# Optimization experiments

Hardware: AMD Instinct MI355X
Metric: run time of the kernel (lower is better)

The kernel has to match this reference:

```python
import jax, jax.numpy as jnp
from jax import lax
import numpy as np

STATE_DIM, LATENT_DIM, HIDDEN_DIM = 18, 3, 16
BN_EPS = 1e-5


def _xavier(key, out_dim, in_dim):
    a = (6.0 / (in_dim + out_dim)) ** 0.5
    return jax.random.uniform(key, (out_dim, in_dim), minval=-a, maxval=a, dtype=jnp.float32)


def setup_inputs() -> dict:
    key = jax.random.key(0)
    ks = jax.random.split(key, 12)
    B, S, T = 4096, 256, 64
    inp = {
        "x_sequence": jax.random.normal(ks[0], (B, S, STATE_DIM), dtype=jnp.float32),
        "t_span": jnp.linspace(0.0, 6.3, T, dtype=jnp.float32),
        # encoder: Linear(18->16), ReLU, (Dropout off), BatchNorm1d(16, eval), Linear(16->3)
        "enc_w1": _xavier(ks[1], HIDDEN_DIM, STATE_DIM), "enc_b1": jnp.zeros((HIDDEN_DIM,), jnp.float32),
        "enc_bn_g": jnp.ones((HIDDEN_DIM,), jnp.float32), "enc_bn_b": jnp.zeros((HIDDEN_DIM,), jnp.float32),
        "enc_bn_m": jnp.zeros((HIDDEN_DIM,), jnp.float32), "enc_bn_v": jnp.ones((HIDDEN_DIM,), jnp.float32),
        "enc_w2": _xavier(ks[2], LATENT_DIM, HIDDEN_DIM), "enc_b2": jnp.zeros((LATENT_DIM,), jnp.float32),
        # decoder: Linear(3->16), ReLU, BN(16, eval), Linear(16->18)
        "dec_w1": _xavier(ks[3], HIDDEN_DIM, LATENT_DIM), "dec_b1": jnp.zeros((HIDDEN_DIM,), jnp.float32),
        "dec_bn_g": jnp.ones((HIDDEN_DIM,), jnp.float32), "dec_bn_b": jnp.zeros((HIDDEN_DIM,), jnp.float32),
        "dec_bn_m": jnp.zeros((HIDDEN_DIM,), jnp.float32), "dec_bn_v": jnp.ones((HIDDEN_DIM,), jnp.float32),
        "dec_w2": _xavier(ks[4], STATE_DIM, HIDDEN_DIM), "dec_b2": jnp.zeros((STATE_DIM,), jnp.float32),
        # ode_func: Linear(3->8), Tanh, Linear(8->3)
        "ode_w1": _xavier(ks[5], HIDDEN_DIM // 2, LATENT_DIM), "ode_b1": jnp.zeros((HIDDEN_DIM // 2,), jnp.float32),
        "ode_w2": _xavier(ks[6], LATENT_DIM, HIDDEN_DIM // 2), "ode_b2": jnp.zeros((LATENT_DIM,), jnp.float32),
        # perturbation classifier: Linear(3->4), ReLU, Linear(4->1), Sigmoid
        "cls_w1": _xavier(ks[7], 4, LATENT_DIM), "cls_b1": jnp.zeros((4,), jnp.float32),
        "cls_w2": _xavier(ks[8], 1, 4), "cls_b2": jnp.zeros((1,), jnp.float32),
    }
    return inp


def _bn_eval(x, g, b, m, v):
    return (x - m) * (g / jnp.sqrt(v + BN_EPS)) + b


def reference(x_sequence, t_span,
              enc_w1, enc_b1, enc_bn_g, enc_bn_b, enc_bn_m, enc_bn_v, enc_w2, enc_b2,
              dec_w1, dec_b1, dec_bn_g, dec_bn_b, dec_bn_m, dec_bn_v, dec_w2, dec_b2,
              ode_w1, ode_b1, ode_w2, ode_b2,
              cls_w1, cls_b1, cls_w2, cls_b2):
    B, S, D = x_sequence.shape
    T = t_span.shape[0]

    def encode(x):  # [N, 18] -> [N, 3]
        h = jax.nn.relu(x @ enc_w1.T + enc_b1)
        h = _bn_eval(h, enc_bn_g, enc_bn_b, enc_bn_m, enc_bn_v)
        return h @ enc_w2.T + enc_b2

    def decode(z):  # [N, 3] -> [N, 18]
        h = jax.nn.relu(z @ dec_w1.T + dec_b1)
        h = _bn_eval(h, dec_bn_g, dec_bn_b, dec_bn_m, dec_bn_v)
        return h @ dec_w2.T + dec_b2

    def ode_func(z):  # [B, 3] -> [B, 3]
        return jnp.tanh(z @ ode_w1.T + ode_b1) @ ode_w2.T + ode_b2

    x_flat = x_sequence.reshape(-1, D)              # [B*S, 18]
    z_flat = encode(x_flat)                         # [B*S, 3]
    z_seq = z_flat.reshape(B, S, LATENT_DIM)
    z0 = z_seq[:, -1, :]                            # [B, 3]

    # explicit Euler integration: z <- z + 0.1 * f(z), T steps
    def step(z, _):
        z_next = z + 0.1 * ode_func(z)
        return z_next, z_next

    _, z_traj = lax.scan(step, z0, None, length=T)  # [T, B, 3]
    z_pred = jnp.transpose(z_traj, (1, 0, 2))       # [B, T, 3]

    x_recon = decode(z_flat).reshape(B, S, D)
    x_pred = decode(z_pred.reshape(-1, LATENT_DIM)).reshape(B, T, D)

    z_mean = jnp.mean(z_seq, axis=1)                # [B, 3]
    h = jax.nn.relu(z_mean @ cls_w1.T + cls_b1)
    perturbation_prob = jax.nn.sigmoid(h @ cls_w2.T + cls_b2)  # [B, 1]

    return (x_recon, x_pred, perturbation_prob, z_seq)
```

## Files before the change

kernel.cpp:

```cpp
#include <hip/hip_runtime.h>
#include <math.h>

constexpr int Bn = 4096, Sn = 256, Tn = 64;
constexpr int Dn = 18, Hn = 16, Ln = 3;
constexpr float EPS = 1e-5f;
constexpr int R = 4;

constexpr size_t OFF_XP   = (size_t)Bn * Sn * Dn;
constexpr size_t OFF_PROB = OFF_XP + (size_t)Bn * Tn * Dn;
constexpr size_t OFF_ZS   = OFF_PROB + (size_t)Bn;

__device__ __forceinline__ float fast_tanh(float x) {
    float ax = fabsf(x);
    float e  = __expf(-2.0f * ax);
    float r  = (1.0f - e) / (1.0f + e);
    return copysignf(r, x);
}

__global__ __launch_bounds__(256) void k1_encdec(
    const float* __restrict__ x,
    const float* __restrict__ ew1, const float* __restrict__ eb1,
    const float* __restrict__ eg,  const float* __restrict__ ebb,
    const float* __restrict__ em,  const float* __restrict__ ev,
    const float* __restrict__ ew2, const float* __restrict__ eb2,
    const float* __restrict__ dw1, const float* __restrict__ db1,
    const float* __restrict__ dg,  const float* __restrict__ dbn,
    const float* __restrict__ dm,  const float* __restrict__ dv,
    const float* __restrict__ dw2, const float* __restrict__ db2,
    const float* __restrict__ cw1, const float* __restrict__ cb1,
    const float* __restrict__ cw2, const float* __restrict__ cb2,
    float* __restrict__ xrec, float* __restrict__ prob, float* __restrict__ zseq)
{
    const int s = threadIdx.x;
    const size_t row0 = (size_t)blockIdx.x * (R * Sn) + s;

    float h[R][Hn];
    #pragma unroll
    for (int j = 0; j < Hn; ++j) {
        float b = eb1[j];
        #pragma unroll
        for (int r = 0; r < R; ++r) h[r][j] = b;
    }
    #pragma unroll
    for (int kk = 0; kk < Dn / 2; ++kk) {
        float2 xa[R];
        #pragma unroll
        for (int r = 0; r < R; ++r)
            xa[r] = *reinterpret_cast<const float2*>(x + (row0 + (size_t)r * Sn) * Dn + 2 * kk);
        #pragma unroll
        for (int j = 0; j < Hn; ++j) {
            float w0 = ew1[j * Dn + 2 * kk];
            float w1 = ew1[j * Dn + 2 * kk + 1];
            #pragma unroll
            for (int r = 0; r < R; ++r) {
                h[r][j] = fmaf(w0, xa[r].x, h[r][j]);
                h[r][j] = fmaf(w1, xa[r].y, h[r][j]);
            }
        }
    }
    #pragma unroll
    for (int j = 0; j < Hn; ++j) {
        float sc = eg[j] / sqrtf(ev[j] + EPS);
        float sh = ebb[j] - em[j] * sc;
        #pragma unroll
        for (int r = 0; r < R; ++r)
            h[r][j] = fmaf(fmaxf(h[r][j], 0.0f), sc, sh);
    }

    float zz[R][Ln];
    #pragma unroll
    for (int c = 0; c < Ln; ++c) {
        float b = eb2[c];
        #pragma unroll
        for (int r = 0; r < R; ++r) zz[r][c] = b;
    }
    #pragma unroll
    for (int j = 0; j < Hn; ++j) {
        #pragma unroll
        for (int c = 0; c < Ln; ++c) {
            float w = ew2[c * Hn + j];
            #pragma unroll
            for (int r = 0; r < R; ++r) zz[r][c] = fmaf(w, h[r][j], zz[r][c]);
        }
    }
    #pragma unroll
    for (int r = 0; r < R; ++r) {
        float* zp = zseq + (row0 + (size_t)r * Sn) * Ln;
        zp[0] = zz[r][0]; zp[1] = zz[r][1]; zp[2] = zz[r][2];
    }

    float h2[R][Hn];
    #pragma unroll
    for (int j = 0; j < Hn; ++j) {
        float w0 = dw1[j * Ln + 0], w1 = dw1[j * Ln + 1], w2 = dw1[j * Ln + 2];
        float b  = db1[j];
        float sc = dg[j] / sqrtf(dv[j] + EPS);
        float sh = dbn[j] - dm[j] * sc;
        #pragma unroll
        for (int r = 0; r < R; ++r) {
            float a = fmaf(w0, zz[r][0], b);
            a = fmaf(w1, zz[r][1], a);
            a = fmaf(w2, zz[r][2], a);
            h2[r][j] = fmaf(fmaxf(a, 0.0f), sc, sh);
        }
    }
    #pragma unroll
    for (int m = 0; m < Dn; m += 2) {
        float o0[R], o1[R];
        #pragma unroll
        for (int r = 0; r < R; ++r) { o0[r] = db2[m]; o1[r] = db2[m + 1]; }
        #pragma unroll
        for (int j = 0; j < Hn; ++j) {
            float wa = dw2[m * Hn + j];
            float wb = dw2[(m + 1) * Hn + j];
            #pragma unroll
            for (int r = 0; r < R; ++r) {
                o0[r] = fmaf(wa, h2[r][j], o0[r]);
                o1[r] = fmaf(wb, h2[r][j], o1[r]);
            }
        }
        #pragma unroll
        for (int r = 0; r < R; ++r)
            *reinterpret_cast<float2*>(xrec + (row0 + (size_t)r * Sn) * Dn + m) =
                make_float2(o0[r], o1[r]);
    }

    float acc[R][Ln];
    #pragma unroll
    for (int r = 0; r < R; ++r)
        #pragma unroll
        for (int c = 0; c < Ln; ++c) acc[r][c] = zz[r][c];
    #pragma unroll
    for (int off = 32; off > 0; off >>= 1) {
        #pragma unroll
        for (int r = 0; r < R; ++r)
            #pragma unroll
            for (int c = 0; c < Ln; ++c)
                acc[r][c] += __shfl_down(acc[r][c], off);
    }
    __shared__ float red[4][R][Ln];
    const int lane = s & 63, wid = s >> 6;
    if (lane == 0) {
        #pragma unroll
        for (int r = 0; r < R; ++r)
            #pragma unroll
            for (int c = 0; c < Ln; ++c) red[wid][r][c] = acc[r][c];
    }
    __syncthreads();
    if (s < R) {
        float m0 = (red[0][s][0] + red[1][s][0] + red[2][s][0] + red[3][s][0]) * (1.0f / Sn);
        float m1 = (red[0][s][1] + red[1][s][1] + red[2][s][1] + red[3][s][1]) * (1.0f / Sn);
        float m2 = (red[0][s][2] + red[1][s][2] + red[2][s][2] + red[3][s][2]) * (1.0f / Sn);
        float logit = cb2[0];
        #pragma unroll
        for (int j = 0; j < 4; ++j) {
            float a = fmaf(cw1[j * 3 + 0], m0, cb1[j]);
            a = fmaf(cw1[j * 3 + 1], m1, a);
            a = fmaf(cw1[j * 3 + 2], m2, a);
            a = fmaxf(a, 0.0f);
            logit = fmaf(cw2[j], a, logit);
        }
        prob[blockIdx.x * R + s] = 1.0f / (1.0f + __expf(-logit));
    }
}

__global__ __launch_bounds__(64) void k2_ode(
    const float* __restrict__ zseq,
    const float* __restrict__ ow1, const float* __restrict__ ob1,
    const float* __restrict__ ow2, const float* __restrict__ ob2,
    float* __restrict__ zscr, int zlayout)
{
    const int b = blockIdx.x * blockDim.x + threadIdx.x;
    const float* zp = zseq + ((size_t)b * Sn + (Sn - 1)) * Ln;
    float z0 = zp[0], z1 = zp[1], z2 = zp[2];

    float w1[8][3], bb1[8], w2v[3][8], bb2[3];
    #pragma unroll
    for (int j = 0; j < 8; ++j) {
        bb1[j] = ob1[j];
        #pragma unroll
        for (int k = 0; k < 3; ++k) w1[j][k] = ow1[j * 3 + k];
    }
    #pragma unroll
    for (int i = 0; i < 3; ++i) {
        bb2[i] = ob2[i];
        #pragma unroll
        for (int j = 0; j < 8; ++j) w2v[i][j] = ow2[i * 8 + j];
    }

    for (int t = 0; t < Tn; ++t) {
        float a[8];
        #pragma unroll
        for (int j = 0; j < 8; ++j) {
            float u = fmaf(w1[j][0], z0, bb1[j]);
            u = fmaf(w1[j][1], z1, u);
            u = fmaf(w1[j][2], z2, u);
            a[j] = fast_tanh(u);
        }
        float d0 = bb2[0], d1 = bb2[1], d2 = bb2[2];
        #pragma unroll
        for (int j = 0; j < 8; ++j) {
            d0 = fmaf(w2v[0][j], a[j], d0);
            d1 = fmaf(w2v[1][j], a[j], d1);
            d2 = fmaf(w2v[2][j], a[j], d2);
        }
        z0 = fmaf(0.1f, d0, z0);
        z1 = fmaf(0.1f, d1, z1);
        z2 = fmaf(0.1f, d2, z2);
        size_t idx = (zlayout == 0) ? ((size_t)t * Bn + b) * Ln
                                    : ((size_t)b * Tn + t) * Dn;
        zscr[idx + 0] = z0; zscr[idx + 1] = z1; zscr[idx + 2] = z2;
    }
}

__global__ __launch_bounds__(256) void k3_decpred(
    const float* __restrict__ dw1, const float* __restrict__ db1,
    const float* __restrict__ dg,  const float* __restrict__ dbn,
    const float* __restrict__ dm,  const float* __restrict__ dv,
    const float* __restrict__ dw2, const float* __restrict__ db2,
    const float* __restrict__ zscr, int zlayout,
    float* __restrict__ xpred)
{
    const int s = threadIdx.x;
    const size_t row0 = (size_t)blockIdx.x * (R * 256) + s;

    float zz[R][Ln];
    #pragma unroll
    for (int r = 0; r < R; ++r) {
        size_t row = row0 + (size_t)r * 256;
        size_t zidx = (zlayout == 0) ? (((row & 63) * Bn + (row >> 6)) * Ln)
                                     : row * Dn;
        zz[r][0] = zscr[zidx + 0];
        zz[r][1] = zscr[zidx + 1];
        zz[r][2] = zscr[zidx + 2];
    }

    float h2[R][Hn];
    #pragma unroll
    for (int j = 0; j < Hn; ++j) {
        float w0 = dw1[j * Ln + 0], w1 = dw1[j * Ln + 1], w2 = dw1[j * Ln + 2];
        float b  = db1[j];
        float sc = dg[j] / sqrtf(dv[j] + EPS);
        float sh = dbn[j] - dm[j] * sc;
        #pragma unroll
        for (int r = 0; r < R; ++r) {
            float a = fmaf(w0, zz[r][0], b);
            a = fmaf(w1, zz[r][1], a);
            a = fmaf(w2, zz[r][2], a);
            h2[r][j] = fmaf(fmaxf(a, 0.0f), sc, sh);
        }
    }
    #pragma unroll
    for (int m = 0; m < Dn; m += 2) {
        float o0[R], o1[R];
        #pragma unroll
        for (int r = 0; r < R; ++r) { o0[r] = db2[m]; o1[r] = db2[m + 1]; }
        #pragma unroll
        for (int j = 0; j < Hn; ++j) {
            float wa = dw2[m * Hn + j];
            float wb = dw2[(m + 1) * Hn + j];
            #pragma unroll
            for (int r = 0; r < R; ++r) {
                o0[r] = fmaf(wa, h2[r][j], o0[r]);
                o1[r] = fmaf(wb, h2[r][j], o1[r]);
            }
        }
        #pragma unroll
        for (int r = 0; r < R; ++r)
            *reinterpret_cast<float2*>(xpred + (row0 + (size_t)r * 256) * Dn + m) =
                make_float2(o0[r], o1[r]);
    }
}

extern "C" void kernel_launch(void* const* d_in, const int* in_sizes, int n_in,
                              void* d_out, int out_size, void* d_ws, size_t ws_size,
                              hipStream_t stream)
{
    const float* x   = (const float*)d_in[0];
    const float* ew1 = (const float*)d_in[2];
    const float* eb1 = (const float*)d_in[3];
    const float* eg  = (const float*)d_in[4];
    const float* ebb = (const float*)d_in[5];
    const float* em  = (const float*)d_in[6];
    const float* ev  = (const float*)d_in[7];
    const float* ew2 = (const float*)d_in[8];
    const float* eb2 = (const float*)d_in[9];
    const float* dw1 = (const float*)d_in[10];
    const float* db1 = (const float*)d_in[11];
    const float* dg  = (const float*)d_in[12];
    const float* dbn = (const float*)d_in[13];
    const float* dm  = (const float*)d_in[14];
    const float* dv  = (const float*)d_in[15];
    const float* dw2 = (const float*)d_in[16];
    const float* db2 = (const float*)d_in[17];
    const float* ow1 = (const float*)d_in[18];
    const float* ob1 = (const float*)d_in[19];
    const float* ow2 = (const float*)d_in[20];
    const float* ob2 = (const float*)d_in[21];
    const float* cw1 = (const float*)d_in[22];
    const float* cb1 = (const float*)d_in[23];
    const float* cw2 = (const float*)d_in[24];
    const float* cb2 = (const float*)d_in[25];

    float* out   = (float*)d_out;
    float* xrec  = out;
    float* xpred = out + OFF_XP;
    float* prob  = out + OFF_PROB;
    float* zseq  = out + OFF_ZS;

    const size_t zbytes = (size_t)Bn * Tn * Ln * sizeof(float);
    float* zscr; int zlayout;
    if (ws_size >= zbytes) { zscr = (float*)d_ws; zlayout = 0; }
    else                   { zscr = xpred;        zlayout = 1; }

    k1_encdec<<<dim3(Bn / R), dim3(Sn), 0, stream>>>(
        x, ew1, eb1, eg, ebb, em, ev, ew2, eb2,
        dw1, db1, dg, dbn, dm, dv, dw2, db2,
        cw1, cb1, cw2, cb2, xrec, prob, zseq);

    k2_ode<<<dim3(Bn / 64), dim3(64), 0, stream>>>(
        zseq, ow1, ob1, ow2, ob2, zscr, zlayout);

    k3_decpred<<<dim3((Bn * Tn) / (R * 256)), dim3(256), 0, stream>>>(
        dw1, db1, dg, dbn, dm, dv, dw2, db2, zscr, zlayout, xpred);
}
```

Baseline: 293.3 us.

## Stage input and output tiles through LDS for coalesced float4 global access

The encoder kernel now loads its whole 4x256x18 input tile into shared memory with coalesced float4 reads. It computes from LDS, writes the reconstruction back into the same buffer, and stores it with coalesced float4 writes. The predicted-decode kernel likewise stages its outputs in LDS before a float4 store. The z scratch layout becomes batch-major with a stride, so the ODE writes and decoder reads are contiguous per row. The cost is about 72KB of LDS per block, which limits occupancy, plus bank conflicts on the stride-18 LDS accesses.

```diff
diff --git a/kernel.cpp b/kernel.cpp
--- a/kernel.cpp
+++ b/kernel.cpp
@@ -32,7 +32,19 @@
     float* __restrict__ xrec, float* __restrict__ prob, float* __restrict__ zseq)
 {
     const int s = threadIdx.x;
-    const size_t row0 = (size_t)blockIdx.x * (R * Sn) + s;
+    constexpr int TILE_F   = Sn * Dn;
+    constexpr int TILE4_F  = R * TILE_F;
+    constexpr int TILE4_F4 = TILE4_F / 4;
+
+    __shared__ float xt[TILE4_F];
+    __shared__ float red[4][R][Ln];
+
+    const size_t base = (size_t)blockIdx.x * TILE4_F;
+    const float4* xg  = reinterpret_cast<const float4*>(x + base);
+    float4*       xt4 = reinterpret_cast<float4*>(xt);
+    #pragma unroll 4
+    for (int i = s; i < TILE4_F4; i += 256) xt4[i] = xg[i];
+    __syncthreads();
 
     float h[R][Hn];
     #pragma unroll
@@ -46,7 +58,7 @@
         float2 xa[R];
         #pragma unroll
         for (int r = 0; r < R; ++r)
-            xa[r] = *reinterpret_cast<const float2*>(x + (row0 + (size_t)r * Sn) * Dn + 2 * kk);
+            xa[r] = *reinterpret_cast<const float2*>(&xt[r * TILE_F + s * Dn + 2 * kk]);
         #pragma unroll
         for (int j = 0; j < Hn; ++j) {
             float w0 = ew1[j * Dn + 2 * kk];
@@ -85,7 +97,7 @@
     }
     #pragma unroll
     for (int r = 0; r < R; ++r) {
-        float* zp = zseq + (row0 + (size_t)r * Sn) * Ln;
+        float* zp = zseq + (((size_t)blockIdx.x * R + r) * Sn + s) * Ln;
         zp[0] = zz[r][0]; zp[1] = zz[r][1]; zp[2] = zz[r][2];
     }
 
@@ -120,10 +132,16 @@
             }
         }
         #pragma unroll
-        for (int r = 0; r < R; ++r)
-            *reinterpret_cast<float2*>(xrec + (row0 + (size_t)r * Sn) * Dn + m) =
-                make_float2(o0[r], o1[r]);
-    }
+        for (int r = 0; r < R; ++r) {
+            xt[r * TILE_F + s * Dn + m]     = o0[r];
+            xt[r * TILE_F + s * Dn + m + 1] = o1[r];
+        }
+    }
+    __syncthreads();
+
+    float4* og = reinterpret_cast<float4*>(xrec + base);
+    #pragma unroll 4
+    for (int i = s; i < TILE4_F4; i += 256) og[i] = xt4[i];
 
     float acc[R][Ln];
     #pragma unroll
@@ -138,7 +156,6 @@
             for (int c = 0; c < Ln; ++c)
                 acc[r][c] += __shfl_down(acc[r][c], off);
     }
-    __shared__ float red[4][R][Ln];
     const int lane = s & 63, wid = s >> 6;
     if (lane == 0) {
         #pragma unroll
@@ -168,7 +185,7 @@
     const float* __restrict__ zseq,
     const float* __restrict__ ow1, const float* __restrict__ ob1,
     const float* __restrict__ ow2, const float* __restrict__ ob2,
-    float* __restrict__ zscr, int zlayout)
+    float* __restrict__ zscr, int zstride)
 {
     const int b = blockIdx.x * blockDim.x + threadIdx.x;
     const float* zp = zseq + ((size_t)b * Sn + (Sn - 1)) * Ln;
@@ -188,6 +205,7 @@
         for (int j = 0; j < 8; ++j) w2v[i][j] = ow2[i * 8 + j];
     }
 
+    float* op = zscr + (size_t)b * Tn * zstride;
     for (int t = 0; t < Tn; ++t) {
         float a[8];
         #pragma unroll
@@ -207,9 +225,7 @@
         z0 = fmaf(0.1f, d0, z0);
         z1 = fmaf(0.1f, d1, z1);
         z2 = fmaf(0.1f, d2, z2);
-        size_t idx = (zlayout == 0) ? ((size_t)t * Bn + b) * Ln
-                                    : ((size_t)b * Tn + t) * Dn;
-        zscr[idx + 0] = z0; zscr[idx + 1] = z1; zscr[idx + 2] = z2;
+        op[t * zstride + 0] = z0; op[t * zstride + 1] = z1; op[t * zstride + 2] = z2;
     }
 }
 
@@ -218,18 +234,22 @@
     const float* __restrict__ dg,  const float* __restrict__ dbn,
     const float* __restrict__ dm,  const float* __restrict__ dv,
     const float* __restrict__ dw2, const float* __restrict__ db2,
-    const float* __restrict__ zscr, int zlayout,
+    const float* __restrict__ zscr, int zstride,
     float* __restrict__ xpred)
 {
     const int s = threadIdx.x;
-    const size_t row0 = (size_t)blockIdx.x * (R * 256) + s;
+    constexpr int ROWS    = R * 256;
+    constexpr int TILE_F  = ROWS * Dn;
+    constexpr int TILE_F4 = TILE_F / 4;
+
+    __shared__ float ot[TILE_F];
+
+    const size_t row0 = (size_t)blockIdx.x * ROWS + s;
 
     float zz[R][Ln];
     #pragma unroll
     for (int r = 0; r < R; ++r) {
-        size_t row = row0 + (size_t)r * 256;
-        size_t zidx = (zlayout == 0) ? (((row & 63) * Bn + (row >> 6)) * Ln)
-                                     : row * Dn;
+        size_t zidx = (row0 + (size_t)r * 256) * zstride;
         zz[r][0] = zscr[zidx + 0];
         zz[r][1] = zscr[zidx + 1];
         zz[r][2] = zscr[zidx + 2];
@@ -266,10 +286,17 @@
             }
         }
         #pragma unroll
-        for (int r = 0; r < R; ++r)
-            *reinterpret_cast<float2*>(xpred + (row0 + (size_t)r * 256) * Dn + m) =
-                make_float2(o0[r], o1[r]);
-    }
+        for (int r = 0; r < R; ++r) {
+            ot[(r * 256 + s) * Dn + m]     = o0[r];
+            ot[(r * 256 + s) * Dn + m + 1] = o1[r];
+        }
+    }
+    __syncthreads();
+
+    float4* og = reinterpret_cast<float4*>(xpred + (size_t)blockIdx.x * TILE_F);
+    const float4* ot4 = reinterpret_cast<const float4*>(ot);
+    #pragma unroll 4
+    for (int i = s; i < TILE_F4; i += 256) og[i] = ot4[i];
 }
 
 extern "C" void kernel_launch(void* const* d_in, const int* in_sizes, int n_in,
@@ -309,9 +336,9 @@
     float* zseq  = out + OFF_ZS;
 
     const size_t zbytes = (size_t)Bn * Tn * Ln * sizeof(float);
-    float* zscr; int zlayout;
-    if (ws_size >= zbytes) { zscr = (float*)d_ws; zlayout = 0; }
-    else                   { zscr = xpred;        zlayout = 1; }
+    float* zscr; int zstride;
+    if (ws_size >= zbytes) { zscr = (float*)d_ws; zstride = Ln; }
+    else                   { zscr = xpred;        zstride = Dn; }
 
     k1_encdec<<<dim3(Bn / R), dim3(Sn), 0, stream>>>(
         x, ew1, eb1, eg, ebb, em, ev, ew2, eb2,
@@ -319,8 +346,8 @@
         cw1, cb1, cw2, cb2, xrec, prob, zseq);
 
     k2_ode<<<dim3(Bn / 64), dim3(64), 0, stream>>>(
-        zseq, ow1, ob1, ow2, ob2, zscr, zlayout);
+        zseq, ow1, ob1, ow2, ob2, zscr, zstride);
 
     k3_decpred<<<dim3((Bn * Tn) / (R * 256)), dim3(256), 0, stream>>>(
-        dw1, db1, dg, dbn, dm, dv, dw2, db2, zscr, zlayout, xpred);
-}
+        dw1, db1, dg, dbn, dm, dv, dw2, db2, zscr, zstride, xpred);
+}
```

Measured after the change: 273.0 us. -6.9%, faster.

## Give each thread four consecutive rows with float4 loads and stores

Applied to the files above, without the earlier changes.

The encoder/decoder kernels now assign four contiguous rows to each thread instead of rows strided by 256. This lets each thread load and store its 72-float row group with float4 vector accesses. The ODE scratch layout changes to batch-major so the predicted-trajectory decoder can also read latents with float4 loads. Loops are reordered to fuse the hidden layer into the output accumulation, and the classifier reduction now uses one wavefront per batch element with no shared memory or barrier. The trade-off is much higher register pressure from 72-element input and output arrays, plus per-lane accesses strided by 288 bytes within a wavefront, which may hurt occupancy and coalescing.

```diff
diff --git a/kernel.cpp b/kernel.cpp
--- a/kernel.cpp
+++ b/kernel.cpp
@@ -4,11 +4,12 @@
 constexpr int Bn = 4096, Sn = 256, Tn = 64;
 constexpr int Dn = 18, Hn = 16, Ln = 3;
 constexpr float EPS = 1e-5f;
-constexpr int R = 4;
 
 constexpr size_t OFF_XP   = (size_t)Bn * Sn * Dn;
 constexpr size_t OFF_PROB = OFF_XP + (size_t)Bn * Tn * Dn;
 constexpr size_t OFF_ZS   = OFF_PROB + (size_t)Bn;
+
+#define OF(e) out_[(e) / Dn][(e) % Dn]
 
 __device__ __forceinline__ float fast_tanh(float x) {
     float ax = fabsf(x);
@@ -32,125 +33,102 @@
     float* __restrict__ xrec, float* __restrict__ prob, float* __restrict__ zseq)
 {
     const int s = threadIdx.x;
-    const size_t row0 = (size_t)blockIdx.x * (R * Sn) + s;
-
-    float h[R][Hn];
-    #pragma unroll
-    for (int j = 0; j < Hn; ++j) {
-        float b = eb1[j];
-        #pragma unroll
-        for (int r = 0; r < R; ++r) h[r][j] = b;
-    }
-    #pragma unroll
-    for (int kk = 0; kk < Dn / 2; ++kk) {
-        float2 xa[R];
-        #pragma unroll
-        for (int r = 0; r < R; ++r)
-            xa[r] = *reinterpret_cast<const float2*>(x + (row0 + (size_t)r * Sn) * Dn + 2 * kk);
-        #pragma unroll
-        for (int j = 0; j < Hn; ++j) {
-            float w0 = ew1[j * Dn + 2 * kk];
-            float w1 = ew1[j * Dn + 2 * kk + 1];
-            #pragma unroll
-            for (int r = 0; r < R; ++r) {
-                h[r][j] = fmaf(w0, xa[r].x, h[r][j]);
-                h[r][j] = fmaf(w1, xa[r].y, h[r][j]);
-            }
-        }
-    }
-    #pragma unroll
-    for (int j = 0; j < Hn; ++j) {
-        float sc = eg[j] / sqrtf(ev[j] + EPS);
-        float sh = ebb[j] - em[j] * sc;
-        #pragma unroll
-        for (int r = 0; r < R; ++r)
-            h[r][j] = fmaf(fmaxf(h[r][j], 0.0f), sc, sh);
-    }
-
-    float zz[R][Ln];
+    const size_t rowBase = (size_t)blockIdx.x * 1024 + 4 * (size_t)s;
+
+    float xv[72];
+    {
+        const float4* xg = reinterpret_cast<const float4*>(x + rowBase * Dn);
+        #pragma unroll
+        for (int i = 0; i < 18; ++i) {
+            float4 t = xg[i];
+            xv[4*i+0] = t.x; xv[4*i+1] = t.y; xv[4*i+2] = t.z; xv[4*i+3] = t.w;
+        }
+    }
+
+    float zz[4][Ln];
     #pragma unroll
     for (int c = 0; c < Ln; ++c) {
         float b = eb2[c];
         #pragma unroll
-        for (int r = 0; r < R; ++r) zz[r][c] = b;
-    }
-    #pragma unroll
+        for (int r = 0; r < 4; ++r) zz[r][c] = b;
+    }
+    #pragma unroll 2
     for (int j = 0; j < Hn; ++j) {
-        #pragma unroll
-        for (int c = 0; c < Ln; ++c) {
-            float w = ew2[c * Hn + j];
+        const float* wr = ew1 + j * Dn;
+        float w[Dn];
+        #pragma unroll
+        for (int k = 0; k < Dn; ++k) w[k] = wr[k];
+        float bj  = eb1[j];
+        float scj = eg[j] / sqrtf(ev[j] + EPS);
+        float shj = ebb[j] - em[j] * scj;
+        float e0 = ew2[0 * Hn + j], e1 = ew2[1 * Hn + j], e2 = ew2[2 * Hn + j];
+        #pragma unroll
+        for (int r = 0; r < 4; ++r) {
+            float a = bj;
             #pragma unroll
-            for (int r = 0; r < R; ++r) zz[r][c] = fmaf(w, h[r][j], zz[r][c]);
-        }
-    }
-    #pragma unroll
-    for (int r = 0; r < R; ++r) {
-        float* zp = zseq + (row0 + (size_t)r * Sn) * Ln;
-        zp[0] = zz[r][0]; zp[1] = zz[r][1]; zp[2] = zz[r][2];
-    }
-
-    float h2[R][Hn];
-    #pragma unroll
+            for (int k = 0; k < Dn; ++k) a = fmaf(w[k], xv[r * Dn + k], a);
+            a = fmaf(fmaxf(a, 0.0f), scj, shj);
+            zz[r][0] = fmaf(e0, a, zz[r][0]);
+            zz[r][1] = fmaf(e1, a, zz[r][1]);
+            zz[r][2] = fmaf(e2, a, zz[r][2]);
+        }
+    }
+
+    {
+        float4* zp4 = reinterpret_cast<float4*>(zseq + rowBase * Ln);
+        zp4[0] = make_float4(zz[0][0], zz[0][1], zz[0][2], zz[1][0]);
+        zp4[1] = make_float4(zz[1][1], zz[1][2], zz[2][0], zz[2][1]);
+        zp4[2] = make_float4(zz[2][2], zz[3][0], zz[3][1], zz[3][2]);
+    }
+
+    float out_[4][Dn];
+    #pragma unroll
+    for (int m = 0; m < Dn; ++m) {
+        float b = db2[m];
+        #pragma unroll
+        for (int r = 0; r < 4; ++r) out_[r][m] = b;
+    }
+    #pragma unroll 2
     for (int j = 0; j < Hn; ++j) {
         float w0 = dw1[j * Ln + 0], w1 = dw1[j * Ln + 1], w2 = dw1[j * Ln + 2];
-        float b  = db1[j];
-        float sc = dg[j] / sqrtf(dv[j] + EPS);
-        float sh = dbn[j] - dm[j] * sc;
-        #pragma unroll
-        for (int r = 0; r < R; ++r) {
-            float a = fmaf(w0, zz[r][0], b);
+        float bj  = db1[j];
+        float scj = dg[j] / sqrtf(dv[j] + EPS);
+        float shj = dbn[j] - dm[j] * scj;
+        float wc[Dn];
+        #pragma unroll
+        for (int m = 0; m < Dn; ++m) wc[m] = dw2[m * Hn + j];
+        #pragma unroll
+        for (int r = 0; r < 4; ++r) {
+            float a = fmaf(w0, zz[r][0], bj);
             a = fmaf(w1, zz[r][1], a);
             a = fmaf(w2, zz[r][2], a);
-            h2[r][j] = fmaf(fmaxf(a, 0.0f), sc, sh);
-        }
-    }
-    #pragma unroll
-    for (int m = 0; m < Dn; m += 2) {
-        float o0[R], o1[R];
-        #pragma unroll
-        for (int r = 0; r < R; ++r) { o0[r] = db2[m]; o1[r] = db2[m + 1]; }
-        #pragma unroll
-        for (int j = 0; j < Hn; ++j) {
-            float wa = dw2[m * Hn + j];
-            float wb = dw2[(m + 1) * Hn + j];
+            a = fmaf(fmaxf(a, 0.0f), scj, shj);
             #pragma unroll
-            for (int r = 0; r < R; ++r) {
-                o0[r] = fmaf(wa, h2[r][j], o0[r]);
-                o1[r] = fmaf(wb, h2[r][j], o1[r]);
-            }
-        }
-        #pragma unroll
-        for (int r = 0; r < R; ++r)
-            *reinterpret_cast<float2*>(xrec + (row0 + (size_t)r * Sn) * Dn + m) =
-                make_float2(o0[r], o1[r]);
-    }
-
-    float acc[R][Ln];
-    #pragma unroll
-    for (int r = 0; r < R; ++r)
-        #pragma unroll
-        for (int c = 0; c < Ln; ++c) acc[r][c] = zz[r][c];
+            for (int m = 0; m < Dn; ++m) out_[r][m] = fmaf(wc[m], a, out_[r][m]);
+        }
+    }
+
+    {
+        float4* og = reinterpret_cast<float4*>(xrec + rowBase * Dn);
+        #pragma unroll
+        for (int i = 0; i < 18; ++i) {
+            int e = 4 * i;
+            og[i] = make_float4(OF(e), OF(e + 1), OF(e + 2), OF(e + 3));
+        }
+    }
+
+    float a0 = zz[0][0] + zz[1][0] + zz[2][0] + zz[3][0];
+    float a1 = zz[0][1] + zz[1][1] + zz[2][1] + zz[3][1];
+    float a2 = zz[0][2] + zz[1][2] + zz[2][2] + zz[3][2];
     #pragma unroll
     for (int off = 32; off > 0; off >>= 1) {
-        #pragma unroll
-        for (int r = 0; r < R; ++r)
-            #pragma unroll
-            for (int c = 0; c < Ln; ++c)
-                acc[r][c] += __shfl_down(acc[r][c], off);
-    }
-    __shared__ float red[4][R][Ln];
+        a0 += __shfl_down(a0, off);
+        a1 += __shfl_down(a1, off);
+        a2 += __shfl_down(a2, off);
+    }
     const int lane = s & 63, wid = s >> 6;
     if (lane == 0) {
-        #pragma unroll
-        for (int r = 0; r < R; ++r)
-            #pragma unroll
-            for (int c = 0; c < Ln; ++c) red[wid][r][c] = acc[r][c];
-    }
-    __syncthreads();
-    if (s < R) {
-        float m0 = (red[0][s][0] + red[1][s][0] + red[2][s][0] + red[3][s][0]) * (1.0f / Sn);
-        float m1 = (red[0][s][1] + red[1][s][1] + red[2][s][1] + red[3][s][1]) * (1.0f / Sn);
-        float m2 = (red[0][s][2] + red[1][s][2] + red[2][s][2] + red[3][s][2]) * (1.0f / Sn);
+        float m0 = a0 * (1.0f / Sn), m1 = a1 * (1.0f / Sn), m2 = a2 * (1.0f / Sn);
         float logit = cb2[0];
         #pragma unroll
         for (int j = 0; j < 4; ++j) {
@@ -160,7 +138,7 @@
             a = fmaxf(a, 0.0f);
             logit = fmaf(cw2[j], a, logit);
         }
-        prob[blockIdx.x * R + s] = 1.0f / (1.0f + __expf(-logit));
+        prob[blockIdx.x * 4 + wid] = 1.0f / (1.0f + __expf(-logit));
     }
 }
 
@@ -168,7 +146,7 @@
     const float* __restrict__ zseq,
     const float* __restrict__ ow1, const float* __restrict__ ob1,
     const float* __restrict__ ow2, const float* __restrict__ ob2,
-    float* __restrict__ zscr, int zlayout)
+    float* __restrict__ zscr, int zstride)
 {
     const int b = blockIdx.x * blockDim.x + threadIdx.x;
     const float* zp = zseq + ((size_t)b * Sn + (Sn - 1)) * Ln;
@@ -188,6 +166,7 @@
         for (int j = 0; j < 8; ++j) w2v[i][j] = ow2[i * 8 + j];
     }
 
+    float* op = zscr + (size_t)b * Tn * zstride;
     for (int t = 0; t < Tn; ++t) {
         float a[8];
         #pragma unroll
@@ -207,9 +186,9 @@
         z0 = fmaf(0.1f, d0, z0);
         z1 = fmaf(0.1f, d1, z1);
         z2 = fmaf(0.1f, d2, z2);
-        size_t idx = (zlayout == 0) ? ((size_t)t * Bn + b) * Ln
-                                    : ((size_t)b * Tn + t) * Dn;
-        zscr[idx + 0] = z0; zscr[idx + 1] = z1; zscr[idx + 2] = z2;
+        op[t * zstride + 0] = z0;
+        op[t * zstride + 1] = z1;
+        op[t * zstride + 2] = z2;
     }
 }
 
@@ -218,57 +197,61 @@
     const float* __restrict__ dg,  const float* __restrict__ dbn,
     const float* __restrict__ dm,  const float* __restrict__ dv,
     const float* __restrict__ dw2, const float* __restrict__ db2,
-    const float* __restrict__ zscr, int zlayout,
+    const float* __restrict__ zscr, int zstride,
     float* __restrict__ xpred)
 {
     const int s = threadIdx.x;
-    const size_t row0 = (size_t)blockIdx.x * (R * 256) + s;
-
-    float zz[R][Ln];
-    #pragma unroll
-    for (int r = 0; r < R; ++r) {
-        size_t row = row0 + (size_t)r * 256;
-        size_t zidx = (zlayout == 0) ? (((row & 63) * Bn + (row >> 6)) * Ln)
-                                     : row * Dn;
-        zz[r][0] = zscr[zidx + 0];
-        zz[r][1] = zscr[zidx + 1];
-        zz[r][2] = zscr[zidx + 2];
-    }
-
-    float h2[R][Hn];
-    #pragma unroll
+    const size_t rowBase = (size_t)blockIdx.x * 1024 + 4 * (size_t)s;
+
+    float zz[4][Ln];
+    if (zstride == Ln) {
+        const float4* zp4 = reinterpret_cast<const float4*>(zscr + rowBase * Ln);
+        float4 t0 = zp4[0], t1 = zp4[1], t2 = zp4[2];
+        zz[0][0] = t0.x; zz[0][1] = t0.y; zz[0][2] = t0.z; zz[1][0] = t0.w;
+        zz[1][1] = t1.x; zz[1][2] = t1.y; zz[2][0] = t1.z; zz[2][1] = t1.w;
+        zz[2][2] = t2.x; zz[3][0] = t2.y; zz[3][1] = t2.z; zz[3][2] = t2.w;
+    } else {
+        #pragma unroll
+        for (int r = 0; r < 4; ++r) {
+            size_t zidx = (rowBase + r) * (size_t)zstride;
+            zz[r][0] = zscr[zidx + 0];
+            zz[r][1] = zscr[zidx + 1];
+            zz[r][2] = zscr[zidx + 2];
+        }
+    }
+
+    float out_[4][Dn];
+    #pragma unroll
+    for (int m = 0; m < Dn; ++m) {
+        float b = db2[m];
+        #pragma unroll
+        for (int r = 0; r < 4; ++r) out_[r][m] = b;
+    }
+    #pragma unroll 2
     for (int j = 0; j < Hn; ++j) {
         float w0 = dw1[j * Ln + 0], w1 = dw1[j * Ln + 1], w2 = dw1[j * Ln + 2];
-        float b  = db1[j];
-        float sc = dg[j] / sqrtf(dv[j] + EPS);
-        float sh = dbn[j] - dm[j] * sc;
-        #pragma unroll
-        for (int r = 0; r < R; ++r) {
-            float a = fmaf(w0, zz[r][0], b);
+        float bj  = db1[j];
+        float scj = dg[j] / sqrtf(dv[j] + EPS);
+        float shj = dbn[j] - dm[j] * scj;
+        float wc[Dn];
+        #pragma unroll
+        for (int m = 0; m < Dn; ++m) wc[m] = dw2[m * Hn + j];
+        #pragma unroll
+        for (int r = 0; r < 4; ++r) {
+            float a = fmaf(w0, zz[r][0], bj);
             a = fmaf(w1, zz[r][1], a);
             a = fmaf(w2, zz[r][2], a);
-            h2[r][j] = fmaf(fmaxf(a, 0.0f), sc, sh);
-        }
-    }
-    #pragma unroll
-    for (int m = 0; m < Dn; m += 2) {
-        float o0[R], o1[R];
-        #pragma unroll
-        for (int r = 0; r < R; ++r) { o0[r] = db2[m]; o1[r] = db2[m + 1]; }
-        #pragma unroll
-        for (int j = 0; j < Hn; ++j) {
-            float wa = dw2[m * Hn + j];
-            float wb = dw2[(m + 1) * Hn + j];
+            a = fmaf(fmaxf(a, 0.0f), scj, shj);
             #pragma unroll
-            for (int r = 0; r < R; ++r) {
-                o0[r] = fmaf(wa, h2[r][j], o0[r]);
-                o1[r] = fmaf(wb, h2[r][j], o1[r]);
-            }
-        }
-        #pragma unroll
-        for (int r = 0; r < R; ++r)
-            *reinterpret_cast<float2*>(xpred + (row0 + (size_t)r * 256) * Dn + m) =
-                make_float2(o0[r], o1[r]);
+            for (int m = 0; m < Dn; ++m) out_[r][m] = fmaf(wc[m], a, out_[r][m]);
+        }
+    }
+
+    float4* og = reinterpret_cast<float4*>(xpred + rowBase * Dn);
+    #pragma unroll
+    for (int i = 0; i < 18; ++i) {
+        int e = 4 * i;
+        og[i] = make_float4(OF(e), OF(e + 1), OF(e + 2), OF(e + 3));
     }
 }
 
@@ -309,18 +292,18 @@
     float* zseq  = out + OFF_ZS;
 
     const size_t zbytes = (size_t)Bn * Tn * Ln * sizeof(float);
-    float* zscr; int zlayout;
-    if (ws_size >= zbytes) { zscr = (float*)d_ws; zlayout = 0; }
-    else                   { zscr = xpred;        zlayout = 1; }
-
-    k1_encdec<<<dim3(Bn / R), dim3(Sn), 0, stream>>>(
+    float* zscr; int zstride;
+    if (ws_size >= zbytes) { zscr = (float*)d_ws; zstride = Ln; }
+    else                   { zscr = xpred;        zstride = Dn; }
+
+    k1_encdec<<<dim3(Bn * Sn / 1024), dim3(256), 0, stream>>>(
         x, ew1, eb1, eg, ebb, em, ev, ew2, eb2,
         dw1, db1, dg, dbn, dm, dv, dw2, db2,
         cw1, cb1, cw2, cb2, xrec, prob, zseq);
 
     k2_ode<<<dim3(Bn / 64), dim3(64), 0, stream>>>(
-        zseq, ow1, ob1, ow2, ob2, zscr, zlayout);
-
-    k3_decpred<<<dim3((Bn * Tn) / (R * 256)), dim3(256), 0, stream>>>(
-        dw1, db1, dg, dbn, dm, dv, dw2, db2, zscr, zlayout, xpred);
-}
+        zseq, ow1, ob1, ow2, ob2, zscr, zstride);
+
+    k3_decpred<<<dim3(Bn * Tn / 1024), dim3(256), 0, stream>>>(
+        dw1, db1, dg, dbn, dm, dv, dw2, db2, zscr, zstride, xpred);
+}
```

Result: faster. 262.9 us (-10.3%).
